# Kernel optimization log

Measured on AMD Instinct MI355X. Metric: run time of the kernel, lower is better.

Reference implementation:

```python
import jax, jax.numpy as jnp
import numpy as np

Cin, E, L, M, H, Cout = 256, 16, 64, 64, 64, 256
B, N = 16, 2048
D = M + L * E  # hypernetwork input dim = 1088


def setup_inputs() -> dict:
    key = jax.random.key(0)
    ks = jax.random.split(key, 8)
    def lin(k, fan_in, shape):
        return jax.random.normal(k, shape, jnp.float32) / np.float32(np.sqrt(fan_in))
    return {
        "x0": jax.random.randint(ks[0], (B, N), 0, Cin),
        "emb": jax.random.normal(ks[1], (Cin, E), jnp.float32) * 0.02,
        "W_enc_w": lin(ks[2], D, (D, H)), "W_enc_b": jnp.zeros((H,), jnp.float32),
        "W_dec_w": lin(ks[3], H, (H, M * M)), "W_dec_b": jnp.zeros((M * M,), jnp.float32),
        "b_enc_w": lin(ks[4], D, (D, H)), "b_enc_b": jnp.zeros((H,), jnp.float32),
        "b_dec_w": lin(ks[5], H, (H, M)), "b_dec_b": jnp.zeros((M,), jnp.float32),
        "dec_w": lin(ks[6], M, (M, Cout)), "dec_b": jnp.zeros((Cout,), jnp.float32),
    }


def reference(x0, emb, W_enc_w, W_enc_b, W_dec_w, W_dec_b,
              b_enc_w, b_enc_b, b_dec_w, b_dec_b, dec_w, dec_b):
    Bq, Nq = x0.shape
    inv_ln2 = jnp.float32(1.0 / np.log(2.0))
    # left-pad with token id 0 (torch pad on int indices pads zeros -> embedding row 0)
    xp = jnp.concatenate([jnp.zeros((Bq, L), x0.dtype), x0], axis=-1)  # [B, N+L]
    e = emb[xp]  # [B, N+L, E]
    # window for step t = tokens t-L..t-1 of x0 = xp[:, t:t+L]
    idxs = jnp.arange(Nq)[:, None] + jnp.arange(L)[None, :]  # [N, L]
    win = e[:, idxs].reshape(Bq, Nq, L * E).transpose(1, 0, 2)  # [N, B, L*E]
    ys = x0.T  # [N, B]

    def mlp(x, ew, eb, dw, db):
        return jax.nn.sigmoid(x @ ew + eb) @ dw + db

    def step(m, xy):
        w, y = xy  # w: [B, L*E], y: [B]
        inp = jnp.concatenate([m, w], axis=-1)  # [B, M + L*E]
        Wm = mlp(inp, W_enc_w, W_enc_b, W_dec_w, W_dec_b).reshape(Bq, M, M)
        bm = mlp(inp, b_enc_w, b_enc_b, b_dec_w, b_dec_b)  # [B, M]
        m = jax.nn.sigmoid(jnp.einsum('bij,bj->bi', Wm, m) + bm)
        logits = m @ dec_w + dec_b  # [B, Cout]
        lse = jax.nn.log_softmax(logits)
        loss = -jnp.take_along_axis(lse, y[:, None], axis=1)[:, 0] * inv_ln2
        return m, loss

    m0 = jnp.zeros((Bq, M), jnp.float32)
    _, losses = jax.lax.scan(step, m0, (win, ys))  # losses: [N, B]
    return losses.reshape(-1)  # matches torch.cat(losses): time-major [N*B]
```

## Files before the change

kernel.cpp:

```cpp
#include <hip/hip_runtime.h>
#include <hip/hip_bf16.h>
#include <hip/hip_fp16.h>


typedef unsigned int uint_t;
typedef unsigned short us_t;
typedef unsigned long long u64_t;
typedef _Float16 h2_t __attribute__((ext_vector_type(2)));

__device__ __forceinline__ us_t f2bf(float f) {
    uint_t u = __float_as_uint(f);
    uint_t r = u + 0x7fffu + ((u >> 16) & 1u);
    return (us_t)(r >> 16);
}
__device__ __forceinline__ float bflo(uint_t u) { return __uint_as_float(u << 16); }
__device__ __forceinline__ float bfhi(uint_t u) { return __uint_as_float(u & 0xffff0000u); }

__device__ __forceinline__ us_t f2h(float f) {
    __half h = __float2half(f);
    return *reinterpret_cast<us_t*>(&h);
}
__device__ __forceinline__ float h2f(us_t s) {
    __half h = *reinterpret_cast<__half*>(&s);
    return __half2float(h);
}
__device__ __forceinline__ h2_t u2h2(uint_t u) {
    union { uint_t u; h2_t h; } x; x.u = u; return x.h;
}

#if __has_builtin(__builtin_amdgcn_fdot2)
__device__ __forceinline__ float dot2f(uint_t a, uint_t b, float c) {
    return __builtin_amdgcn_fdot2(u2h2(a), u2h2(b), c, false);
}
#else
__device__ __forceinline__ float dot2f(uint_t a, uint_t b, float c) {
    h2_t x = u2h2(a), y = u2h2(b);
    return c + (float)x.x * (float)y.x + (float)x.y * (float)y.y;
}
#endif

#define DOT4(q, base, acc)                                              \
    acc = dot2f(q.x, mreg2u[(base) + 0], acc);                          \
    acc = dot2f(q.y, mreg2u[(base) + 1], acc);                          \
    acc = dot2f(q.z, mreg2u[(base) + 2], acc);                          \
    acc = dot2f(q.w, mreg2u[(base) + 3], acc);

__global__ void cvt_kernel(const float* __restrict__ Wdecw,
                           const float* __restrict__ decw,
                           const float* __restrict__ Wencw,
                           const float* __restrict__ bencw,
                           us_t* __restrict__ WdG, us_t* __restrict__ decwY,
                           us_t* __restrict__ EWmG) {
    int o = blockIdx.x * 256 + threadIdx.x;
    if (o < 262144) {
        int s = o >> 16;
        int idx = o & 65535;
        int k = idx & 7;
        int oo = (idx >> 3) & 1023;
        int jp = idx >> 13;
        int h = s * 16 + (oo >> 6);
        int i = oo & 63;
        int j = jp * 8 + k;
        WdG[o] = f2h(Wdecw[h * 4096 + i * 64 + j]);
    } else if (o < 278528) {
        int oo = o - 262144;
        int k = oo & 3, lane = (oo >> 2) & 63, mm = oo >> 8;
        decwY[oo] = f2bf(decw[mm * 256 + k * 64 + lane]);
    } else if (o < 286720) {
        int oo = o - 278528;
        int kk = oo & 7, h2 = (oo >> 3) & 127, jp = oo >> 10;
        int j = jp * 8 + kk;
        float v = (h2 < 64) ? Wencw[j * 64 + h2] : bencw[j * 64 + (h2 - 64)];
        EWmG[oo] = f2h(v);
    }
}

__global__ void build_T(const float* __restrict__ emb, const float* __restrict__ Wencw,
                        const float* __restrict__ bencw, float* __restrict__ T) {
    int l = blockIdx.x >> 8, v = blockIdx.x & 255, h2 = threadIdx.x;
    float acc = 0.f;
#pragma unroll
    for (int e = 0; e < 16; ++e) {
        int d = 64 + l * 16 + e;
        float w = (h2 < 64) ? Wencw[d * 64 + h2] : bencw[d * 64 + (h2 - 64)];
        acc += emb[v * 16 + e] * w;
    }
    T[blockIdx.x * 128 + h2] = acc;
}

__global__ void build_P(const float* __restrict__ T, const int* __restrict__ x0,
                        const float* __restrict__ Wencb, const float* __restrict__ bencb,
                        float* __restrict__ P) {
    int t = blockIdx.x >> 4, b = blockIdx.x & 15, h2 = threadIdx.x;
    float acc = (h2 < 64) ? Wencb[h2] : bencb[h2 - 64];
    for (int l = 0; l < 64; ++l) {
        int p = t + l;
        int v = (p < 64) ? 0 : x0[b * 2048 + (p - 64)];
        acc += T[(l * 256 + v) * 128 + h2];
    }
    P[blockIdx.x * 128 + h2] = acc;
}

__global__ __launch_bounds__(512, 2) void recur(
    const float* __restrict__ bdecw, const float* __restrict__ bdecb,
    const float* __restrict__ Wdecb, const us_t* __restrict__ WdG,
    const us_t* __restrict__ EWmG, const float* __restrict__ P,
    uint_t* __restrict__ mh32, u64_t* __restrict__ pxb) {
    const int b = blockIdx.x & 15, s = blockIdx.x >> 4;
    const int tid = threadIdx.x;

    extern __shared__ char smem[];
    us_t*   EWm2   = (us_t*)(smem);
    uint_t* wdbt2  = (uint_t*)(smem + 16384);
    uint_t* bdec2  = (uint_t*)(smem + 24576);
    float*  V_s    = (float*)(smem + 32768);
    float*  rp4_s  = (float*)(smem + 36928);
    float*  wdbm2_s= (float*)(smem + 37952);
    float*  hbb2_s = (float*)(smem + 38464);
    float*  hw_s   = (float*)(smem + 38976);
    uint_t* hb2_s  = (uint_t*)(smem + 39232);
    uint_t* m2_s   = (uint_t*)(smem + 39360);
    float*  bias_s = (float*)(smem + 39488);

    uint4 wreg[16];
    {
        const uint4* g4 = (const uint4*)WdG + s * 8192;
#pragma unroll
        for (int jp = 0; jp < 8; ++jp) {
            wreg[jp]     = g4[jp * 1024 + tid];
            wreg[8 + jp] = g4[jp * 1024 + tid + 512];
        }
    }
    {
        const uint4* g4 = (const uint4*)EWmG;
        uint4* l4 = (uint4*)EWm2;
        for (int k = tid; k < 1024; k += 512) l4[k] = g4[k];
    }
    for (int k = tid; k < 2048; k += 512) {
        int jj = k >> 6, i = k & 63;
        wdbt2[k] = (uint_t)f2h(Wdecb[i * 64 + 2 * jj])
                 | ((uint_t)f2h(Wdecb[i * 64 + 2 * jj + 1]) << 16);
        bdec2[k] = (uint_t)f2h(bdecw[(2 * jj) * 64 + i])
                 | ((uint_t)f2h(bdecw[(2 * jj + 1) * 64 + i]) << 16);
    }
    if (tid < 64) bias_s[tid] = bdecb[tid];
    if (tid < 32) m2_s[tid] = 0u;
    __syncthreads();

    uint_t mreg2u[32];
#pragma unroll
    for (int j = 0; j < 32; ++j) mreg2u[j] = 0u;

    float preg = 0.f;
    if (tid < 128) preg = P[b * 128 + tid];

    const uint4* EW4 = (const uint4*)EWm2;
    const int hl = tid >> 6, iA = tid & 63;
    const int w = tid >> 6;

    for (int t = 0; t < 2048; ++t) {
        float pnext = 0.f;
        int tp = (t < 2047) ? (t + 1) : 2047;
        if (tid < 128) pnext = P[(tp * 16 + b) * 128 + tid];

        float a0 = 0.f, a1 = 0.f;
#pragma unroll
        for (int jp = 0; jp < 8; ++jp) {
            uint4 q0 = wreg[jp];
            uint4 q1 = wreg[8 + jp];
            DOT4(q0, jp * 4, a0);
            DOT4(q1, jp * 4, a1);
        }
        V_s[hl * 65 + iA] = a0;
        V_s[(hl + 8) * 65 + iA] = a1;

        if (tid < 128) {
            float acc = preg;
#pragma unroll
            for (int jp = 0; jp < 8; ++jp) {
                uint4 e = EW4[jp * 128 + tid];
                DOT4(e, jp * 4, acc);
            }
            float sg = 1.f / (1.f + __expf(-acc));
            if (tid < 64) {
                hw_s[tid] = sg;
            } else {
                int l = tid - 64;
                float vlo = __shfl(sg, (l & 31) * 2, 64);
                float vhi = __shfl(sg, (l & 31) * 2 + 1, 64);
                if (l < 32)
                    hb2_s[l] = (uint_t)f2h(vlo) | ((uint_t)f2h(vhi) << 16);
            }
        }
        preg = pnext;
        __syncthreads();

        u64_t* slotb = pxb + (u64_t)(((t & 1) * 16 + b) * 4) * 64;
        const uint_t tg = (uint_t)(t + 1);

        if (tid < 64) {
            float r0 = 0.f, r1 = 0.f;
#pragma unroll
            for (int hh = 0; hh < 8; ++hh) {
                r0 += hw_s[s * 16 + 2 * hh]     * V_s[(2 * hh) * 65 + tid];
                r1 += hw_s[s * 16 + 2 * hh + 1] * V_s[(2 * hh + 1) * 65 + tid];
            }
            float rs = r0 + r1;
            rp4_s[s * 64 + tid] = rs;
            u64_t pay = ((u64_t)tg << 32) | (u64_t)__float_as_uint(rs);
            __hip_atomic_store(slotb + s * 64 + tid, pay,
                               __ATOMIC_RELAXED, __HIP_MEMORY_SCOPE_AGENT);
        }

        if (w < 3) {
            int p = w + (w >= s ? 1 : 0);
            int lane = tid & 63;
            const u64_t* src = slotb + p * 64 + lane;
            u64_t v;
            for (;;) {
                v = __hip_atomic_load(src, __ATOMIC_RELAXED,
                                      __HIP_MEMORY_SCOPE_AGENT);
                if (__ballot((uint_t)(v >> 32) == tg) == ~0ull) break;
                __builtin_amdgcn_s_sleep(1);
            }
            rp4_s[p * 64 + lane] = __uint_as_float((uint_t)v);
        } else if (w < 5) {
            int i = tid & 63;
            float wm = 0.f, hbv = 0.f;
            if (w == 3) {
#pragma unroll
                for (int jj = 0; jj < 16; ++jj) {
                    wm  = dot2f(wdbt2[jj * 64 + i], mreg2u[jj], wm);
                    hbv = dot2f(bdec2[jj * 64 + i], hb2_s[jj], hbv);
                }
                wdbm2_s[i] = wm;
                hbb2_s[i] = hbv;
            } else {
#pragma unroll
                for (int jj = 0; jj < 16; ++jj) {
                    wm  = dot2f(wdbt2[(16 + jj) * 64 + i], mreg2u[16 + jj], wm);
                    hbv = dot2f(bdec2[(16 + jj) * 64 + i], hb2_s[16 + jj], hbv);
                }
                wdbm2_s[64 + i] = wm;
                hbb2_s[64 + i] = hbv;
            }
        }
        __syncthreads();

        if (tid < 64) {
            float r = ((rp4_s[tid] + rp4_s[64 + tid])
                     + (rp4_s[128 + tid] + rp4_s[192 + tid]))
                    + (wdbm2_s[tid] + wdbm2_s[64 + tid])
                    + (hbb2_s[tid] + hbb2_s[64 + tid])
                    + bias_s[tid];
            float nm = 1.f / (1.f + __expf(-r));
            us_t nh = f2h(nm);
            uint_t nhu = (uint_t)nh;
            uint_t lo = (uint_t)__shfl((int)nhu, (tid & 31) * 2, 64);
            uint_t hi = (uint_t)__shfl((int)nhu, (tid & 31) * 2 + 1, 64);
            if (tid < 32) {
                uint_t pk = lo | (hi << 16);
                m2_s[tid] = pk;
                if (s == 0) mh32[(t * 16 + b) * 32 + tid] = pk;
            }
        }
        __syncthreads();

        {
            const uint4* mg = (const uint4*)m2_s;
#pragma unroll
            for (int p = 0; p < 8; ++p) {
                uint4 v = mg[p];
                mreg2u[p * 4 + 0] = v.x;
                mreg2u[p * 4 + 1] = v.y;
                mreg2u[p * 4 + 2] = v.z;
                mreg2u[p * 4 + 3] = v.w;
            }
        }
    }
}

__global__ __launch_bounds__(256) void loss_kernel(
    const us_t* __restrict__ mhb, const us_t* __restrict__ decwY,
    const float* __restrict__ decb, const int* __restrict__ x0,
    float* __restrict__ out) {
    __shared__ __align__(16) us_t dw[16384];
    const int tid = threadIdx.x;
    {
        const uint4* g4 = (const uint4*)decwY;
        uint4* l4 = (uint4*)dw;
        for (int k = tid; k < 2048; k += 256) l4[k] = g4[k];
    }
    __syncthreads();
    const int lane = tid & 63, wv = tid >> 6;
    const uint2* dwu2 = (const uint2*)dw;
    float b0 = decb[lane], b1 = decb[lane + 64];
    float b2 = decb[lane + 128], b3 = decb[lane + 192];
    for (int r = 0; r < 8; ++r) {
        int row = blockIdx.x * 32 + wv * 8 + r;
        float mL = h2f(mhb[row * 64 + lane]);
        float l0 = b0, l1 = b1, l2 = b2, l3 = b3;
#pragma unroll
        for (int mm = 0; mm < 64; ++mm) {
            float mv = __shfl(mL, mm, 64);
            uint2 q = dwu2[mm * 64 + lane];
            l0 += mv * bflo(q.x);
            l1 += mv * bfhi(q.x);
            l2 += mv * bflo(q.y);
            l3 += mv * bfhi(q.y);
        }
        float mx = fmaxf(fmaxf(l0, l1), fmaxf(l2, l3));
#pragma unroll
        for (int o = 32; o > 0; o >>= 1) mx = fmaxf(mx, __shfl_xor(mx, o, 64));
        float se = __expf(l0 - mx) + __expf(l1 - mx) + __expf(l2 - mx) + __expf(l3 - mx);
#pragma unroll
        for (int o = 32; o > 0; o >>= 1) se += __shfl_xor(se, o, 64);
        float lse = mx + __logf(se);
        int t = row >> 4, bb = row & 15;
        int y = x0[bb * 2048 + t];
        int hi = y >> 6;
        float cand = hi == 0 ? l0 : (hi == 1 ? l1 : (hi == 2 ? l2 : l3));
        float ly = __shfl(cand, y & 63, 64);
        if (lane == 0) out[row] = (lse - ly) * 1.4426950408889634f;
    }
}

extern "C" void kernel_launch(void* const* d_in, const int* in_sizes, int n_in,
                              void* d_out, int out_size, void* d_ws, size_t ws_size,
                              hipStream_t stream) {
    const int*   x0    = (const int*)d_in[0];
    const float* emb   = (const float*)d_in[1];
    const float* Wencw = (const float*)d_in[2];
    const float* Wencb = (const float*)d_in[3];
    const float* Wdecw = (const float*)d_in[4];
    const float* Wdecb = (const float*)d_in[5];
    const float* bencw = (const float*)d_in[6];
    const float* bencb = (const float*)d_in[7];
    const float* bdecw = (const float*)d_in[8];
    const float* bdecb = (const float*)d_in[9];
    const float* decw  = (const float*)d_in[10];
    const float* decb  = (const float*)d_in[11];
    float* out = (float*)d_out;

    char* ws = (char*)d_ws;
    us_t*   WdG   = (us_t*)(ws);
    us_t*   decwY = (us_t*)(ws + 524288);
    us_t*   EWmG  = (us_t*)(ws + 557056);
    u64_t*  pxb   = (u64_t*)(ws + 573440);
    float*  T     = (float*)(ws + 638976);
    uint_t* mh32  = (uint_t*)T;
    float*  P     = (float*)(ws + 9027584);

    static const int kRecurLds = 157632;
    (void)hipFuncSetAttribute((const void*)recur,
                              hipFuncAttributeMaxDynamicSharedMemorySize,
                              kRecurLds);

    cvt_kernel<<<1120, 256, 0, stream>>>(Wdecw, decw, Wencw, bencw,
                                         WdG, decwY, EWmG);
    build_T<<<16384, 128, 0, stream>>>(emb, Wencw, bencw, T);
    build_P<<<32768, 128, 0, stream>>>(T, x0, Wencb, bencb, P);
    (void)hipMemsetAsync(pxb, 0, 65536, stream);
    recur<<<64, 512, kRecurLds, stream>>>(bdecw, bdecb, Wdecb, WdG, EWmG,
                                          P, mh32, pxb);
    loss_kernel<<<1024, 256, 0, stream>>>((const us_t*)mh32, decwY, decb, x0, out);
}
```

Baseline: 3.277 ms.

## Co-locate cooperating blocks per XCC and poll exchange slots via L2

```diff
diff --git a/kernel.cpp b/kernel.cpp
--- a/kernel.cpp
+++ b/kernel.cpp
@@ -44,6 +44,18 @@
     acc = dot2f(q.y, mreg2u[(base) + 1], acc);                          \
     acc = dot2f(q.z, mreg2u[(base) + 2], acc);                          \
     acc = dot2f(q.w, mreg2u[(base) + 3], acc);
+
+__device__ __forceinline__ void l2_store_u64(u64_t* p, u64_t v) {
+    asm volatile("global_store_dwordx2 %0, %1, off"
+                 :: "v"(p), "v"(v) : "memory");
+}
+__device__ __forceinline__ u64_t l2_load_u64(const u64_t* p) {
+    u64_t v;
+    asm volatile("global_load_dwordx2 %0, %1, off sc0\n\t"
+                 "s_waitcnt vmcnt(0)"
+                 : "=v"(v) : "v"(p) : "memory");
+    return v;
+}
 
 __global__ void cvt_kernel(const float* __restrict__ Wdecw,
                            const float* __restrict__ decw,
@@ -105,8 +117,8 @@
     const float* __restrict__ bdecw, const float* __restrict__ bdecb,
     const float* __restrict__ Wdecb, const us_t* __restrict__ WdG,
     const us_t* __restrict__ EWmG, const float* __restrict__ P,
-    uint_t* __restrict__ mh32, u64_t* __restrict__ pxb) {
-    const int b = blockIdx.x & 15, s = blockIdx.x >> 4;
+    uint_t* __restrict__ mh32, u64_t* __restrict__ pxbA,
+    u64_t* __restrict__ pxbL, uint_t* __restrict__ claimed) {
     const int tid = threadIdx.x;
 
     extern __shared__ char smem[];
@@ -121,6 +133,28 @@
     uint_t* hb2_s  = (uint_t*)(smem + 39232);
     uint_t* m2_s   = (uint_t*)(smem + 39360);
     float*  bias_s = (float*)(smem + 39488);
+    int*    role_p = (int*)(smem + 39744);
+
+    if (tid == 0) {
+        uint_t xcc = __builtin_amdgcn_s_getreg((31u << 11) | 20u) & 7u;
+        int role = -1;
+#pragma unroll 1
+        for (int k = 0; k < 8; ++k) {
+            int r = (int)xcc * 8 + k;
+            if (atomicCAS(&claimed[r], 0u, 1u) == 0u) { role = r; break; }
+        }
+        if (role < 0) {
+#pragma unroll 1
+            for (int r = 0; r < 64; ++r)
+                if (atomicCAS(&claimed[r], 0u, 1u) == 0u) { role = r; break; }
+        }
+        *role_p = role;
+    }
+    __syncthreads();
+    const int role = *role_p;
+    if (role < 0) return;
+    const int b = role >> 2;
+    const int s = role & 3;
 
     uint4 wreg[16];
     {
@@ -157,6 +191,7 @@
     const uint4* EW4 = (const uint4*)EWm2;
     const int hl = tid >> 6, iA = tid & 63;
     const int w = tid >> 6;
+    int fastok = 1;
 
     for (int t = 0; t < 2048; ++t) {
         float pnext = 0.f;
@@ -195,7 +230,9 @@
         preg = pnext;
         __syncthreads();
 
-        u64_t* slotb = pxb + (u64_t)(((t & 1) * 16 + b) * 4) * 64;
+        const int slotoff = ((t & 1) * 16 + b) * 4 * 64;
+        u64_t* slotLb = pxbL + slotoff;
+        u64_t* slotAb = pxbA + slotoff;
         const uint_t tg = (uint_t)(t + 1);
 
         if (tid < 64) {
@@ -208,20 +245,34 @@
             float rs = r0 + r1;
             rp4_s[s * 64 + tid] = rs;
             u64_t pay = ((u64_t)tg << 32) | (u64_t)__float_as_uint(rs);
-            __hip_atomic_store(slotb + s * 64 + tid, pay,
+            l2_store_u64(slotLb + s * 64 + tid, pay);
+            __hip_atomic_store(slotAb + s * 64 + tid, pay,
                                __ATOMIC_RELAXED, __HIP_MEMORY_SCOPE_AGENT);
         }
 
         if (w < 3) {
             int p = w + (w >= s ? 1 : 0);
             int lane = tid & 63;
-            const u64_t* src = slotb + p * 64 + lane;
-            u64_t v;
-            for (;;) {
-                v = __hip_atomic_load(src, __ATOMIC_RELAXED,
-                                      __HIP_MEMORY_SCOPE_AGENT);
-                if (__ballot((uint_t)(v >> 32) == tg) == ~0ull) break;
-                __builtin_amdgcn_s_sleep(1);
+            const u64_t* srcL = slotLb + p * 64 + lane;
+            const u64_t* srcA = slotAb + p * 64 + lane;
+            u64_t v; int got = 0;
+            if (fastok) {
+                for (int it = 0; it < 64; ++it) {
+                    v = l2_load_u64(srcL);
+                    if (__ballot((uint_t)(v >> 32) == tg) == ~0ull) {
+                        got = 1; break;
+                    }
+                    __builtin_amdgcn_s_sleep(1);
+                }
+                if (!got) fastok = 0;
+            }
+            if (!got) {
+                for (;;) {
+                    v = __hip_atomic_load(srcA, __ATOMIC_RELAXED,
+                                          __HIP_MEMORY_SCOPE_AGENT);
+                    if (__ballot((uint_t)(v >> 32) == tg) == ~0ull) break;
+                    __builtin_amdgcn_s_sleep(1);
+                }
             }
             rp4_s[p * 64 + lane] = __uint_as_float((uint_t)v);
         } else if (w < 5) {
@@ -346,9 +397,11 @@
     us_t*   WdG   = (us_t*)(ws);
     us_t*   decwY = (us_t*)(ws + 524288);
     us_t*   EWmG  = (us_t*)(ws + 557056);
-    u64_t*  pxb   = (u64_t*)(ws + 573440);
+    u64_t*  pxbA  = (u64_t*)(ws + 573440);
     float*  T     = (float*)(ws + 638976);
     uint_t* mh32  = (uint_t*)T;
+    u64_t*  pxbL  = (u64_t*)(ws + 638976 + 4194304);
+    uint_t* claimed = (uint_t*)(ws + 638976 + 4194304 + 65536);
     float*  P     = (float*)(ws + 9027584);
 
     static const int kRecurLds = 157632;
@@ -360,8 +413,9 @@
                                          WdG, decwY, EWmG);
     build_T<<<16384, 128, 0, stream>>>(emb, Wencw, bencw, T);
     build_P<<<32768, 128, 0, stream>>>(T, x0, Wencb, bencb, P);
-    (void)hipMemsetAsync(pxb, 0, 65536, stream);
-    recur<<<64, 512, kRecurLds, stream>>>(bdecw, bdecb, Wdecb, WdG, EWmG,
-                                          P, mh32, pxb);
+    (void)hipMemsetAsync(pxbA, 0, 65536, stream);
+    (void)hipMemsetAsync(pxbL, 0, 65536 + 256, stream);
+    recur<<<256, 512, kRecurLds, stream>>>(bdecw, bdecb, Wdecb, WdG, EWmG,
+                                           P, mh32, pxbA, pxbL, claimed);
     loss_kernel<<<1024, 256, 0, stream>>>((const us_t*)mh32, decwY, decb, x0, out);
 }
```

After: 3.706 ms. 13.1% more time.
